# Kernel optimization log

Measured on AMD Instinct MI355X. Metric: run time of the kernel, lower is better.

The kernel has to match this reference:

```python
import jax, jax.numpy as jnp
import numpy as np

N = 50000
E = 800000
IN_DIM = 128
HID = 32
HEADS = 4
NEG_SLOPE = 0.2


def setup_inputs() -> dict:
    key = jax.random.key(0)
    ks = jax.random.split(key, 12)
    x = jax.random.normal(ks[0], (N, IN_DIM), dtype=jnp.float32)
    edge_index = jax.random.randint(ks[1], (2, E), 0, N, dtype=jnp.int64)
    s1 = 1.0 / np.sqrt(IN_DIM)
    s2 = 1.0 / np.sqrt(HEADS * HID)
    W1 = jax.random.normal(ks[2], (IN_DIM, HEADS * HID), dtype=jnp.float32) * s1
    a_src1 = jax.random.normal(ks[3], (HEADS, HID), dtype=jnp.float32) * s1
    a_dst1 = jax.random.normal(ks[4], (HEADS, HID), dtype=jnp.float32) * s1
    b1 = jnp.zeros((HEADS * HID,), dtype=jnp.float32)
    W2 = jax.random.normal(ks[5], (HEADS * HID, HID), dtype=jnp.float32) * s2
    a_src2 = jax.random.normal(ks[6], (1, HID), dtype=jnp.float32) * s2
    a_dst2 = jax.random.normal(ks[7], (1, HID), dtype=jnp.float32) * s2
    b2 = jnp.zeros((HID,), dtype=jnp.float32)
    return {"x": x, "edge_index": edge_index, "W1": W1, "a_src1": a_src1,
            "a_dst1": a_dst1, "b1": b1, "W2": W2, "a_src2": a_src2,
            "a_dst2": a_dst2, "b2": b2}


def _gat_layer(x, W, a_src, a_dst, bias, src, dst, heads, ch):
    n = x.shape[0]
    h = (x @ W).reshape(n, heads, ch)                    # [N,H,C]
    # per-node attention halves (GATv1): a_src . h_i, a_dst . h_j
    al_s = jnp.einsum('nhc,hc->nh', h, a_src)            # [N,H]
    al_d = jnp.einsum('nhc,hc->nh', h, a_dst)
    e = jax.nn.leaky_relu(al_s[src] + al_d[dst], NEG_SLOPE)  # [E,H]
    # segment softmax over edges sharing the same destination
    e_max = jax.ops.segment_max(e, dst, num_segments=n)
    e_exp = jnp.exp(e - e_max[dst])
    denom = jax.ops.segment_sum(e_exp, dst, num_segments=n)
    alpha = e_exp / (denom[dst] + 1e-16)                 # [E,H]
    msg = h[src] * alpha[:, :, None]                     # [E,H,C]
    out = jax.ops.segment_sum(msg, dst, num_segments=n)  # [N,H,C]
    return out.reshape(n, heads * ch) + bias


def reference(x, edge_index, W1, a_src1, a_dst1, b1, W2, a_src2, a_dst2, b2):
    n = x.shape[0]
    # PyG GATConv adds self-loops by default
    loops = jnp.arange(n, dtype=edge_index.dtype)
    src = jnp.concatenate([edge_index[0], loops])
    dst = jnp.concatenate([edge_index[1], loops])
    h = _gat_layer(x, W1, a_src1, a_dst1, b1, src, dst, HEADS, HID)
    h = jax.nn.elu(h)
    out = _gat_layer(h, W2, a_src2, a_dst2, b2, src, dst, 1, HID)
    return out
```

## Files before the change

kernel.cpp:

```cpp
#include <hip/hip_runtime.h>
#include <hip/hip_bf16.h>

#define NN 50000
#define EE 800000
#define EN (EE + NN)
#define IN_DIM 128
#define HID 32
#define HEADS 4
#define F1 (HEADS * HID)
#define NEG 0.2f

typedef __hip_bfloat16 bf16;
typedef __bf16 bf16x8 __attribute__((ext_vector_type(8)));
typedef float f32x4 __attribute__((ext_vector_type(4)));

__device__ __forceinline__ float cvt(float v) { return v; }
__device__ __forceinline__ float cvt(bf16 v)  { return __bfloat162float(v); }

__device__ __forceinline__ float bflo(unsigned u) {
    union { unsigned u; float f; } v; v.u = u << 16; return v.f;
}
__device__ __forceinline__ float bfhi(unsigned u) {
    union { unsigned u; float f; } v; v.u = u & 0xFFFF0000u; return v.f;
}

__device__ __forceinline__ unsigned short f2bf_bits(float f) {
    union { float f; unsigned u; } v; v.f = f;
    unsigned r = v.u + 0x7FFFu + ((v.u >> 16) & 1u);
    return (unsigned short)(r >> 16);
}

__device__ __forceinline__ unsigned short f2h_bits(float f) {
    _Float16 h = (_Float16)f;
    union { _Float16 h; unsigned short s; } v; v.h = h; return v.s;
}
__device__ __forceinline__ float h2f(unsigned short s) {
    union { _Float16 h; unsigned short s; } v; v.s = s; return (float)v.h;
}

__device__ __forceinline__ float rec_exp(uint4 r, int h) {
    unsigned w = (h & 2) ? r.z : r.y;
    unsigned short b = (h & 1) ? (unsigned short)(w >> 16) : (unsigned short)(w & 0xFFFFu);
    return h2f(b);
}

__global__ void k_prep(const void* xv, const void* eiv, const void* W1v, const void* W2v,
                       int* __restrict__ flags,
                       unsigned short* __restrict__ W1T, unsigned short* __restrict__ W2T) {
    __shared__ int sf;
    const int t = threadIdx.x;
    if (t < 64) {
        const unsigned* xw = (const unsigned*)xv;
        const unsigned* ew = (const unsigned*)eiv;
        int lo_nz = 0, huge = 0, hi_nz = 0;
        for (int j = 0; j < 4; ++j) {
            unsigned w = xw[t * 4 + j];
            unsigned lo = w & 0xFFFFu;
            if (lo != 0u) lo_nz = 1;
            if (((lo >> 7) & 0xFFu) >= 0xC0u) huge = 1;
            unsigned eo = ew[(t * 4 + j) * 2 + 1];
            if (eo != 0u) hi_nz = 1;
        }
        unsigned long long m_lo = __ballot(lo_nz);
        unsigned long long m_hg = __ballot(huge);
        unsigned long long m_hi = __ballot(hi_nz);
        if (t == 0) {
            int f0 = (m_lo == 0ull || m_hg != 0ull) ? 1 : 0;
            int f1 = (m_hi == 0ull) ? 1 : 0;
            flags[0] = f0; flags[1] = f1;
            sf = f0;
        }
    }
    __syncthreads();
    const int f32in = sf;
    const unsigned short* w1g = (const unsigned short*)W1v;
    const float* w1f = (const float*)W1v;
    for (int i = 0; i < 64; ++i) {
        int id = i * 256 + t;
        int n = id >> 7, k = id & 127;
        W1T[id] = f32in ? f2bf_bits(w1f[k * 128 + n]) : w1g[k * 128 + n];
    }
    const unsigned short* w2g = (const unsigned short*)W2v;
    const float* w2f = (const float*)W2v;
    for (int i = 0; i < 16; ++i) {
        int id = i * 256 + t;
        int n = id >> 7, k = id & 127;
        W2T[id] = f32in ? f2bf_bits(w2f[k * 32 + n]) : w2g[k * 32 + n];
    }
}

template <typename IT>
__device__ __forceinline__ void get_sd(const IT* __restrict__ ei, int idx, int& s, int& d) {
    if (idx < EE) { s = (int)ei[idx]; d = (int)ei[EE + idx]; }
    else          { s = d = idx - EE; }
}
template <typename IT>
__device__ __forceinline__ int dst_of(const IT* __restrict__ ei, int idx) {
    return idx < EE ? (int)ei[EE + idx] : idx - EE;
}

#define MROWS 64
#define LDK 136

__global__ __launch_bounds__(256) void k_lin1_mfma(
    const void* xv, const unsigned short* __restrict__ W1T,
    const void* as1v, const void* ad1v,
    const int* __restrict__ flags, unsigned* __restrict__ h1,
    float* __restrict__ als, float* __restrict__ ald)
{
    __shared__ __align__(16) char smem[(MROWS + 128) * LDK * 2];
    unsigned short* xs  = (unsigned short*)smem;
    unsigned short* w1t = xs + MROWS * LDK;
    float* hs = (float*)smem;
    __shared__ float sa[F1], sd[F1];

    const int t = threadIdx.x;
    const int row0 = blockIdx.x * MROWS;
    const int f32in = flags[0];

    if (t < F1) {
        sa[t] = f32in ? ((const float*)as1v)[t] : cvt(((const bf16*)as1v)[t]);
        sd[t] = f32in ? ((const float*)ad1v)[t] : cvt(((const bf16*)ad1v)[t]);
    }
    if (!f32in) {
        const uint4* xg = (const uint4*)xv;
        for (int i = 0; i < 4; ++i) {
            int id = i * 256 + t;
            int m = id >> 4, seg = id & 15;
            int gr = row0 + m;
            uint4 val = (gr < NN) ? xg[(size_t)gr * 16 + seg] : make_uint4(0, 0, 0, 0);
            *(uint4*)&xs[m * LDK + seg * 8] = val;
        }
    } else {
        const float* xf = (const float*)xv;
        for (int i = 0; i < 32; ++i) {
            int id = i * 256 + t;
            int m = id >> 7, c = id & 127;
            int gr = row0 + m;
            xs[m * LDK + c] = (gr < NN) ? f2bf_bits(xf[(size_t)gr * 128 + c]) : 0;
        }
    }
    {
        const uint4* wg = (const uint4*)W1T;
        for (int i = 0; i < 8; ++i) {
            int id = i * 256 + t;
            int n = id >> 4, seg = id & 15;
            *(uint4*)&w1t[n * LDK + seg * 8] = wg[id];
        }
    }
    __syncthreads();

    const int wave = t >> 6, lane = t & 63, quad = lane >> 4, l16 = lane & 15;
    f32x4 acc[8];
#pragma unroll
    for (int ni = 0; ni < 8; ++ni) acc[ni] = (f32x4){0.f, 0.f, 0.f, 0.f};

    const int arow = wave * 16 + l16;
#pragma unroll
    for (int kc = 0; kc < 4; ++kc) {
        int ko = kc * 32 + quad * 8;
        bf16x8 av = *(const bf16x8*)&xs[arow * LDK + ko];
#pragma unroll
        for (int ni = 0; ni < 8; ++ni) {
            bf16x8 bv = *(const bf16x8*)&w1t[(ni * 16 + l16) * LDK + ko];
            acc[ni] = __builtin_amdgcn_mfma_f32_16x16x32_bf16(av, bv, acc[ni], 0, 0, 0);
        }
    }
    __syncthreads();

#pragma unroll
    for (int ni = 0; ni < 8; ++ni)
#pragma unroll
        for (int r = 0; r < 4; ++r) {
            int m = wave * 16 + quad * 4 + r;
            hs[m * 132 + ni * 16 + l16] = acc[ni][r];
        }
    __syncthreads();

    for (int i = 0; i < 16; ++i) {
        int id = i * 256 + t;
        int m = id >> 6, wd = id & 63;
        int gr = row0 + m;
        if (gr < NN) {
            unsigned pw = (unsigned)f2bf_bits(hs[m * 132 + 2 * wd]) |
                          ((unsigned)f2bf_bits(hs[m * 132 + 2 * wd + 1]) << 16);
            h1[(size_t)gr * 64 + wd] = pw;
        }
    }
    {
        int m = t >> 2, h = t & 3;
        int gr = row0 + m;
        if (gr < NN) {
            float ps = 0.f, pd = 0.f;
#pragma unroll
            for (int j = 0; j < 32; ++j) {
                float v = hs[m * 132 + h * 32 + j];
                ps += v * sa[h * 32 + j];
                pd += v * sd[h * 32 + j];
            }
            als[gr * 4 + h] = ps;
            ald[gr * 4 + h] = pd;
        }
    }
}

#define SCAN_B 196

__global__ void k_hist(const void* ei, const int* __restrict__ flags,
                       int* __restrict__ counts, int* __restrict__ rank) {
    int idx = blockIdx.x * blockDim.x + threadIdx.x;
    if (idx >= EN) return;
    int d = flags[1] ? dst_of<long long>((const long long*)ei, idx)
                     : dst_of<int>((const int*)ei, idx);
    rank[idx] = atomicAdd(&counts[d], 1);
}

__global__ void k_scanA(const int* __restrict__ counts, int* __restrict__ bsum) {
    __shared__ int sh[256];
    int i = blockIdx.x * 256 + threadIdx.x;
    sh[threadIdx.x] = (i < NN) ? counts[i] : 0;
    __syncthreads();
    for (int off = 128; off > 0; off >>= 1) {
        if (threadIdx.x < off) sh[threadIdx.x] += sh[threadIdx.x + off];
        __syncthreads();
    }
    if (threadIdx.x == 0) bsum[blockIdx.x] = sh[0];
}

__global__ void k_scanC(const int* __restrict__ counts, const int* __restrict__ bsum,
                        int* __restrict__ offsets) {
    __shared__ int red[256];
    __shared__ int sh[256];
    const int t = threadIdx.x, b = blockIdx.x;
    red[t] = (t < b) ? bsum[t] : 0;
    __syncthreads();
    for (int off = 128; off > 0; off >>= 1) {
        if (t < off) red[t] += red[t + off];
        __syncthreads();
    }
    const int base = red[0];
    int i = b * 256 + t;
    int v = (i < NN) ? counts[i] : 0;
    sh[t] = v;
    __syncthreads();
    for (int off = 1; off < 256; off <<= 1) {
        int u = (t >= off) ? sh[t - off] : 0;
        __syncthreads();
        sh[t] += u;
        __syncthreads();
    }
    if (i < NN) {
        offsets[i] = base + sh[t] - v;
    } else if (i == NN) {
        offsets[NN] = EN;
    }
}

__global__ void k_scatter(const void* ei, const int* __restrict__ flags,
                          const int* __restrict__ offsets, const int* __restrict__ rank,
                          const float4* __restrict__ als, const float4* __restrict__ ald,
                          uint4* __restrict__ rec) {
    int idx = blockIdx.x * blockDim.x + threadIdx.x;
    if (idx >= EN) return;
    int s, d;
    if (flags[1]) get_sd<long long>((const long long*)ei, idx, s, d);
    else          get_sd<int>((const int*)ei, idx, s, d);
    int slot = offsets[d] + rank[idx];
    float4 a = als[s], b = ald[d];
    float e0 = a.x + b.x, e1 = a.y + b.y, e2 = a.z + b.z, e3 = a.w + b.w;
    e0 = e0 > 0.f ? e0 : NEG * e0;
    e1 = e1 > 0.f ? e1 : NEG * e1;
    e2 = e2 > 0.f ? e2 : NEG * e2;
    e3 = e3 > 0.f ? e3 : NEG * e3;
    unsigned w0 = (unsigned)f2h_bits(__expf(e0)) | ((unsigned)f2h_bits(__expf(e1)) << 16);
    unsigned w1 = (unsigned)f2h_bits(__expf(e2)) | ((unsigned)f2h_bits(__expf(e3)) << 16);
    rec[slot] = make_uint4((unsigned)s, w0, w1, 0u);
}

__global__ __launch_bounds__(256) void k_agg1(
    const int* __restrict__ offsets, const uint4* __restrict__ rec,
    const bf16* __restrict__ h1, const void* b1v, const int* __restrict__ flags,
    uint2* __restrict__ hm)
{
    const int lane = threadIdx.x & 63;
    const int d = blockIdx.x * 4 + (threadIdx.x >> 6);
    const int q = lane >> 5;
    const int u = lane & 31;
    const int h = u >> 3;
    const int start = offsets[d], end = offsets[d + 1];
    const uint2* rows = (const uint2*)h1;

    float A0[4] = {0,0,0,0}, A1[4] = {0,0,0,0}, A2[4] = {0,0,0,0}, A3[4] = {0,0,0,0};
    float D[4] = {0,0,0,0};
    int e = start + q;
    for (; e + 6 < end; e += 8) {
        uint4 r0 = rec[e],     r1 = rec[e + 2];
        uint4 r2 = rec[e + 4], r3 = rec[e + 6];
        float x0 = rec_exp(r0, h), x1 = rec_exp(r1, h);
        float x2 = rec_exp(r2, h), x3 = rec_exp(r3, h);
        uint2 u0 = rows[r0.x * 32 + u], u1 = rows[r1.x * 32 + u];
        uint2 u2 = rows[r2.x * 32 + u], u3 = rows[r3.x * 32 + u];
        A0[0] += x0 * bflo(u0.x); A0[1] += x0 * bfhi(u0.x);
        A0[2] += x0 * bflo(u0.y); A0[3] += x0 * bfhi(u0.y); D[0] += x0;
        A1[0] += x1 * bflo(u1.x); A1[1] += x1 * bfhi(u1.x);
        A1[2] += x1 * bflo(u1.y); A1[3] += x1 * bfhi(u1.y); D[1] += x1;
        A2[0] += x2 * bflo(u2.x); A2[1] += x2 * bfhi(u2.x);
        A2[2] += x2 * bflo(u2.y); A2[3] += x2 * bfhi(u2.y); D[2] += x2;
        A3[0] += x3 * bflo(u3.x); A3[1] += x3 * bfhi(u3.x);
        A3[2] += x3 * bflo(u3.y); A3[3] += x3 * bfhi(u3.y); D[3] += x3;
    }
    for (; e < end; e += 2) {
        uint4 r0 = rec[e];
        float x0 = rec_exp(r0, h);
        uint2 u0 = rows[r0.x * 32 + u];
        A0[0] += x0 * bflo(u0.x); A0[1] += x0 * bfhi(u0.x);
        A0[2] += x0 * bflo(u0.y); A0[3] += x0 * bfhi(u0.y); D[0] += x0;
    }
    float a0 = A0[0] + A1[0] + A2[0] + A3[0];
    float a1 = A0[1] + A1[1] + A2[1] + A3[1];
    float a2 = A0[2] + A1[2] + A2[2] + A3[2];
    float a3 = A0[3] + A1[3] + A2[3] + A3[3];
    float dsum = D[0] + D[1] + D[2] + D[3];
    a0 += __shfl_xor(a0, 32); a1 += __shfl_xor(a1, 32);
    a2 += __shfl_xor(a2, 32); a3 += __shfl_xor(a3, 32);
    dsum += __shfl_xor(dsum, 32);
    if (q == 0) {
        float inv = 1.f / (dsum + 1e-16f);
        float bb0, bb1, bb2, bb3;
        if (flags[0]) {
            float4 bb = ((const float4*)b1v)[u];
            bb0 = bb.x; bb1 = bb.y; bb2 = bb.z; bb3 = bb.w;
        } else {
            uint2 ub = ((const uint2*)b1v)[u];
            bb0 = bflo(ub.x); bb1 = bfhi(ub.x); bb2 = bflo(ub.y); bb3 = bfhi(ub.y);
        }
        float v0 = a0 * inv + bb0, v1 = a1 * inv + bb1;
        float v2 = a2 * inv + bb2, v3 = a3 * inv + bb3;
        v0 = v0 > 0.f ? v0 : (__expf(v0) - 1.f);
        v1 = v1 > 0.f ? v1 : (__expf(v1) - 1.f);
        v2 = v2 > 0.f ? v2 : (__expf(v2) - 1.f);
        v3 = v3 > 0.f ? v3 : (__expf(v3) - 1.f);
        unsigned w0 = (unsigned)f2bf_bits(v0) | ((unsigned)f2bf_bits(v1) << 16);
        unsigned w1 = (unsigned)f2bf_bits(v2) | ((unsigned)f2bf_bits(v3) << 16);
        hm[(size_t)d * 32 + u] = make_uint2(w0, w1);
    }
}

__global__ __launch_bounds__(256) void k_mid_mfma(
    const bf16* __restrict__ hm, const unsigned short* __restrict__ W2T,
    const void* as2v, const void* ad2v,
    const int* __restrict__ flags, unsigned short* __restrict__ h2,
    float* __restrict__ als2, float* __restrict__ ald2)
{
    __shared__ __align__(16) unsigned short hs[MROWS * LDK];
    __shared__ __align__(16) unsigned short w2t[32 * LDK];
    __shared__ float sa2[HID], sd2[HID];

    const int t = threadIdx.x;
    const int row0 = blockIdx.x * MROWS;
    const int f32in = flags[0];

    if (t < HID) {
        sa2[t] = f32in ? ((const float*)as2v)[t] : cvt(((const bf16*)as2v)[t]);
        sd2[t] = f32in ? ((const float*)ad2v)[t] : cvt(((const bf16*)ad2v)[t]);
    }
    {
        const uint4* hg = (const uint4*)hm;
        for (int i = 0; i < 4; ++i) {
            int id = i * 256 + t;
            int m = id >> 4, seg = id & 15;
            int gr = row0 + m;
            uint4 val = (gr < NN) ? hg[(size_t)gr * 16 + seg] : make_uint4(0, 0, 0, 0);
            *(uint4*)&hs[m * LDK + seg * 8] = val;
        }
        const uint4* wg = (const uint4*)W2T;
        for (int i = 0; i < 2; ++i) {
            int id = i * 256 + t;
            int n = id >> 4, seg = id & 15;
            *(uint4*)&w2t[n * LDK + seg * 8] = wg[id];
        }
    }
    __syncthreads();

    const int wave = t >> 6, lane = t & 63, quad = lane >> 4, l16 = lane & 15;
    f32x4 acc[2];
    acc[0] = (f32x4){0.f, 0.f, 0.f, 0.f};
    acc[1] = (f32x4){0.f, 0.f, 0.f, 0.f};
    const int arow = wave * 16 + l16;
#pragma unroll
    for (int kc = 0; kc < 4; ++kc) {
        int ko = kc * 32 + quad * 8;
        bf16x8 av = *(const bf16x8*)&hs[arow * LDK + ko];
#pragma unroll
        for (int ni = 0; ni < 2; ++ni) {
            bf16x8 bv = *(const bf16x8*)&w2t[(ni * 16 + l16) * LDK + ko];
            acc[ni] = __builtin_amdgcn_mfma_f32_16x16x32_bf16(av, bv, acc[ni], 0, 0, 0);
        }
    }

#pragma unroll
    for (int ni = 0; ni < 2; ++ni)
#pragma unroll
        for (int r = 0; r < 4; ++r) {
            int gr = row0 + wave * 16 + quad * 4 + r;
            if (gr < NN) h2[(size_t)gr * 32 + ni * 16 + l16] = f2h_bits(acc[ni][r]);
        }

    float ps[4], pd[4];
#pragma unroll
    for (int r = 0; r < 4; ++r) {
        ps[r] = acc[0][r] * sa2[l16] + acc[1][r] * sa2[16 + l16];
        pd[r] = acc[0][r] * sd2[l16] + acc[1][r] * sd2[16 + l16];
    }
#pragma unroll
    for (int mask = 1; mask < 16; mask <<= 1)
#pragma unroll
        for (int r = 0; r < 4; ++r) {
            ps[r] += __shfl_xor(ps[r], mask);
            pd[r] += __shfl_xor(pd[r], mask);
        }
    if (l16 == 0) {
#pragma unroll
        for (int r = 0; r < 4; ++r) {
            int gr = row0 + wave * 16 + quad * 4 + r;
            if (gr < NN) { als2[gr] = ps[r]; ald2[gr] = pd[r]; }
        }
    }
}

__global__ __launch_bounds__(256) void k_agg2(
    const int* __restrict__ offsets, const uint4* __restrict__ rec,
    const float* __restrict__ als2, const float* __restrict__ ald2,
    const unsigned* __restrict__ h2,
    const void* b2v, const int* __restrict__ flags, void* out)
{
    const int lane = threadIdx.x & 63;
    const int node = blockIdx.x * 4 + (threadIdx.x >> 6);
    const int q = lane >> 4;
    const int u = lane & 15;
    const int start = offsets[node], end = offsets[node + 1];
    const float adv = ald2[node];

    float A0 = 0.f, A1 = 0.f, B0 = 0.f, B1 = 0.f, D0 = 0.f, D1 = 0.f;
    int e = start + q;
    for (; e + 4 < end; e += 8) {
        int s0 = (int)rec[e].x, s1 = (int)rec[e + 4].x;
        float e0 = als2[s0] + adv, e1 = als2[s1] + adv;
        e0 = e0 > 0.f ? e0 : NEG * e0;
        e1 = e1 > 0.f ? e1 : NEG * e1;
        float x0 = __expf(e0), x1 = __expf(e1);
        unsigned w0 = h2[s0 * 16 + u];
        unsigned w1 = h2[s1 * 16 + u];
        A0 += x0 * h2f((unsigned short)(w0 & 0xFFFFu));
        A1 += x0 * h2f((unsigned short)(w0 >> 16));  D0 += x0;
        B0 += x1 * h2f((unsigned short)(w1 & 0xFFFFu));
        B1 += x1 * h2f((unsigned short)(w1 >> 16));  D1 += x1;
    }
    for (; e < end; e += 4) {
        int s0 = (int)rec[e].x;
        float e0 = als2[s0] + adv;
        e0 = e0 > 0.f ? e0 : NEG * e0;
        float x0 = __expf(e0);
        unsigned w0 = h2[s0 * 16 + u];
        A0 += x0 * h2f((unsigned short)(w0 & 0xFFFFu));
        A1 += x0 * h2f((unsigned short)(w0 >> 16));  D0 += x0;
    }
    float a0 = A0 + B0, a1 = A1 + B1, dsum = D0 + D1;
    a0 += __shfl_xor(a0, 16); a1 += __shfl_xor(a1, 16); dsum += __shfl_xor(dsum, 16);
    a0 += __shfl_xor(a0, 32); a1 += __shfl_xor(a1, 32); dsum += __shfl_xor(dsum, 32);
    if (q == 0) {
        float inv = 1.f / (dsum + 1e-16f);
        float r0 = a0 * inv, r1 = a1 * inv;
        if (flags[0]) {
            float2 bb = ((const float2*)b2v)[u];
            ((float2*)out)[(size_t)node * 16 + u] = make_float2(r0 + bb.x, r1 + bb.y);
        } else {
            unsigned ub = ((const unsigned*)b2v)[u];
            r0 += bflo(ub); r1 += bfhi(ub);
            ((unsigned*)out)[(size_t)node * 16 + u] =
                (unsigned)f2bf_bits(r0) | ((unsigned)f2bf_bits(r1) << 16);
        }
    }
}

extern "C" void kernel_launch(void* const* d_in, const int* in_sizes, int n_in,
                              void* d_out, int out_size, void* d_ws, size_t ws_size,
                              hipStream_t stream) {
    const void* x    = d_in[0];
    const void* ei   = d_in[1];
    const void* W1   = d_in[2];
    const void* a_s1 = d_in[3];
    const void* a_d1 = d_in[4];
    const void* b1   = d_in[5];
    const void* W2   = d_in[6];
    const void* a_s2 = d_in[7];
    const void* a_d2 = d_in[8];
    const void* b2v  = d_in[9];

    int*   flags  = (int*)d_ws;
    char*  pc     = (char*)d_ws + 256;
    uint2* hm     = (uint2*)pc;            pc += (size_t)NN * 32 * 8;
    int*   rank   = (int*)hm;
    bf16*  h1     = (bf16*)pc;             pc += (size_t)NN * F1 * 2;
    unsigned short* h2 = (unsigned short*)h1;
    uint4* rec    = (uint4*)pc;            pc += (size_t)EN * 16;
    float* al_s1  = (float*)pc;            pc += (size_t)NN * HEADS * 4;
    float* al_d1  = (float*)pc;            pc += (size_t)NN * HEADS * 4;
    float* al_s2  = (float*)pc;            pc += (size_t)NN * 4;
    float* al_d2  = (float*)pc;            pc += (size_t)NN * 4;
    int*   offs   = (int*)pc;              pc += (size_t)(NN + 4) * 4;
    int*   counts = (int*)pc;              pc += (size_t)NN * 4;
    unsigned short* W1T = (unsigned short*)pc; pc += (size_t)128 * 128 * 2;
    unsigned short* W2T = (unsigned short*)pc; pc += (size_t)32 * 128 * 2;
    int*   bsum   = (int*)pc;              pc += SCAN_B * 4;

    hipMemsetAsync(counts, 0, (size_t)NN * sizeof(int), stream);

    k_prep<<<1, 256, 0, stream>>>(x, ei, W1, W2, flags, W1T, W2T);
    k_hist<<<(EN + 255) / 256, 256, 0, stream>>>(ei, flags, counts, rank);
    k_scanA<<<SCAN_B, 256, 0, stream>>>(counts, bsum);
    k_scanC<<<SCAN_B, 256, 0, stream>>>(counts, bsum, offs);
    k_lin1_mfma<<<(NN + MROWS - 1) / MROWS, 256, 0, stream>>>(x, W1T, a_s1, a_d1,
                                                              flags, (unsigned*)h1,
                                                              al_s1, al_d1);
    k_scatter<<<(EN + 255) / 256, 256, 0, stream>>>(ei, flags, offs, rank,
                                                    (const float4*)al_s1,
                                                    (const float4*)al_d1, rec);
    k_agg1<<<NN / 4, 256, 0, stream>>>(offs, rec, h1, b1, flags, hm);
    k_mid_mfma<<<(NN + MROWS - 1) / MROWS, 256, 0, stream>>>((const bf16*)hm, W2T, a_s2,
                                                             a_d2, flags, h2, al_s2, al_d2);
    k_agg2<<<NN / 4, 256, 0, stream>>>(offs, rec, al_s2, al_d2, (const unsigned*)h2,
                                       b2v, flags, d_out);
}
```

Before: 261.6 us.

## Pre-pack W1 into MFMA fragment layout and drop LDS staging in lin1

k_prep now writes W1 in the per-lane MFMA B-fragment order, so k_lin1 can load B operands straight from global memory with coalesced uint4 loads. The A fragments are also loaded directly into registers. This removes all LDS staging and syncthreads from the first linear layer. Each block now covers 32 rows, with waves split across row and column halves, and the attention dot products use wave shuffles instead of an LDS pass. The trade-off is scattered 2-byte h1 stores and the W1 fragments being re-read from L2 by every block.

```diff
diff --git a/kernel.cpp b/kernel.cpp
--- a/kernel.cpp
+++ b/kernel.cpp
@@ -46,7 +46,7 @@
 
 __global__ void k_prep(const void* xv, const void* eiv, const void* W1v, const void* W2v,
                        int* __restrict__ flags,
-                       unsigned short* __restrict__ W1T, unsigned short* __restrict__ W2T) {
+                       uint4* __restrict__ W1F, unsigned short* __restrict__ W2T) {
     __shared__ int sf;
     const int t = threadIdx.x;
     if (t < 64) {
@@ -74,11 +74,22 @@
     __syncthreads();
     const int f32in = sf;
     const unsigned short* w1g = (const unsigned short*)W1v;
-    const float* w1f = (const float*)W1v;
-    for (int i = 0; i < 64; ++i) {
-        int id = i * 256 + t;
-        int n = id >> 7, k = id & 127;
-        W1T[id] = f32in ? f2bf_bits(w1f[k * 128 + n]) : w1g[k * 128 + n];
+    const float* w1f32 = (const float*)W1v;
+    for (int i = 0; i < 8; ++i) {
+        int e = i * 256 + t;
+        int nc = e >> 6, lane = e & 63;
+        int ni = nc >> 2, kc = nc & 3, quad = lane >> 4, l16 = lane & 15;
+        int n = ni * 16 + l16, k0 = kc * 32 + quad * 8;
+        unsigned wds[4];
+#pragma unroll
+        for (int p = 0; p < 4; ++p) {
+            unsigned short b0 = f32in ? f2bf_bits(w1f32[(k0 + 2 * p) * 128 + n])
+                                      : w1g[(k0 + 2 * p) * 128 + n];
+            unsigned short b1 = f32in ? f2bf_bits(w1f32[(k0 + 2 * p + 1) * 128 + n])
+                                      : w1g[(k0 + 2 * p + 1) * 128 + n];
+            wds[p] = (unsigned)b0 | ((unsigned)b1 << 16);
+        }
+        W1F[e] = make_uint4(wds[0], wds[1], wds[2], wds[3]);
     }
     const unsigned short* w2g = (const unsigned short*)W2v;
     const float* w2f = (const float*)W2v;
@@ -99,107 +110,103 @@
     return idx < EE ? (int)ei[EE + idx] : idx - EE;
 }
 
-#define MROWS 64
-#define LDK 136
-
 __global__ __launch_bounds__(256) void k_lin1_mfma(
-    const void* xv, const unsigned short* __restrict__ W1T,
+    const void* xv, const uint4* __restrict__ W1F,
     const void* as1v, const void* ad1v,
-    const int* __restrict__ flags, unsigned* __restrict__ h1,
+    const int* __restrict__ flags, unsigned short* __restrict__ h1,
     float* __restrict__ als, float* __restrict__ ald)
 {
-    __shared__ __align__(16) char smem[(MROWS + 128) * LDK * 2];
-    unsigned short* xs  = (unsigned short*)smem;
-    unsigned short* w1t = xs + MROWS * LDK;
-    float* hs = (float*)smem;
-    __shared__ float sa[F1], sd[F1];
-
     const int t = threadIdx.x;
-    const int row0 = blockIdx.x * MROWS;
+    const int w = t >> 6, lane = t & 63, quad = lane >> 4, l16 = lane & 15;
+    const int rhalf = w & 1, chalf = w >> 1;
+    const int row0 = blockIdx.x * 32 + rhalf * 16;
+    const int arow = row0 + l16;
     const int f32in = flags[0];
 
-    if (t < F1) {
-        sa[t] = f32in ? ((const float*)as1v)[t] : cvt(((const bf16*)as1v)[t]);
-        sd[t] = f32in ? ((const float*)ad1v)[t] : cvt(((const bf16*)ad1v)[t]);
-    }
+    uint4 av4[4];
+    const bool okr = arow < NN;
     if (!f32in) {
         const uint4* xg = (const uint4*)xv;
-        for (int i = 0; i < 4; ++i) {
-            int id = i * 256 + t;
-            int m = id >> 4, seg = id & 15;
-            int gr = row0 + m;
-            uint4 val = (gr < NN) ? xg[(size_t)gr * 16 + seg] : make_uint4(0, 0, 0, 0);
-            *(uint4*)&xs[m * LDK + seg * 8] = val;
-        }
+#pragma unroll
+        for (int kc = 0; kc < 4; ++kc)
+            av4[kc] = okr ? xg[(size_t)arow * 16 + kc * 4 + quad]
+                          : make_uint4(0, 0, 0, 0);
     } else {
         const float* xf = (const float*)xv;
-        for (int i = 0; i < 32; ++i) {
-            int id = i * 256 + t;
-            int m = id >> 7, c = id & 127;
-            int gr = row0 + m;
-            xs[m * LDK + c] = (gr < NN) ? f2bf_bits(xf[(size_t)gr * 128 + c]) : 0;
-        }
-    }
-    {
-        const uint4* wg = (const uint4*)W1T;
-        for (int i = 0; i < 8; ++i) {
-            int id = i * 256 + t;
-            int n = id >> 4, seg = id & 15;
-            *(uint4*)&w1t[n * LDK + seg * 8] = wg[id];
-        }
-    }
-    __syncthreads();
-
-    const int wave = t >> 6, lane = t & 63, quad = lane >> 4, l16 = lane & 15;
-    f32x4 acc[8];
-#pragma unroll
-    for (int ni = 0; ni < 8; ++ni) acc[ni] = (f32x4){0.f, 0.f, 0.f, 0.f};
-
-    const int arow = wave * 16 + l16;
+#pragma unroll
+        for (int kc = 0; kc < 4; ++kc) {
+            unsigned wds[4];
+#pragma unroll
+            for (int p = 0; p < 4; ++p) {
+                int k = kc * 32 + quad * 8 + 2 * p;
+                float v0 = okr ? xf[(size_t)arow * 128 + k] : 0.f;
+                float v1 = okr ? xf[(size_t)arow * 128 + k + 1] : 0.f;
+                wds[p] = (unsigned)f2bf_bits(v0) | ((unsigned)f2bf_bits(v1) << 16);
+            }
+            av4[kc] = make_uint4(wds[0], wds[1], wds[2], wds[3]);
+        }
+    }
+
+    f32x4 acc[4];
+#pragma unroll
+    for (int nil = 0; nil < 4; ++nil) acc[nil] = (f32x4){0.f, 0.f, 0.f, 0.f};
 #pragma unroll
     for (int kc = 0; kc < 4; ++kc) {
-        int ko = kc * 32 + quad * 8;
-        bf16x8 av = *(const bf16x8*)&xs[arow * LDK + ko];
-#pragma unroll
-        for (int ni = 0; ni < 8; ++ni) {
-            bf16x8 bv = *(const bf16x8*)&w1t[(ni * 16 + l16) * LDK + ko];
-            acc[ni] = __builtin_amdgcn_mfma_f32_16x16x32_bf16(av, bv, acc[ni], 0, 0, 0);
-        }
-    }
-    __syncthreads();
-
-#pragma unroll
-    for (int ni = 0; ni < 8; ++ni)
+        bf16x8 a = *(bf16x8*)&av4[kc];
+#pragma unroll
+        for (int nil = 0; nil < 4; ++nil) {
+            int nb = chalf * 4 + nil;
+            bf16x8 b = *(const bf16x8*)&W1F[(nb * 4 + kc) * 64 + lane];
+            acc[nil] = __builtin_amdgcn_mfma_f32_16x16x32_bf16(a, b, acc[nil], 0, 0, 0);
+        }
+    }
+
+#pragma unroll
+    for (int nil = 0; nil < 4; ++nil) {
+        int col = (chalf * 4 + nil) * 16 + l16;
 #pragma unroll
         for (int r = 0; r < 4; ++r) {
-            int m = wave * 16 + quad * 4 + r;
-            hs[m * 132 + ni * 16 + l16] = acc[ni][r];
-        }
-    __syncthreads();
-
-    for (int i = 0; i < 16; ++i) {
-        int id = i * 256 + t;
-        int m = id >> 6, wd = id & 63;
-        int gr = row0 + m;
-        if (gr < NN) {
-            unsigned pw = (unsigned)f2bf_bits(hs[m * 132 + 2 * wd]) |
-                          ((unsigned)f2bf_bits(hs[m * 132 + 2 * wd + 1]) << 16);
-            h1[(size_t)gr * 64 + wd] = pw;
-        }
-    }
-    {
-        int m = t >> 2, h = t & 3;
-        int gr = row0 + m;
-        if (gr < NN) {
-            float ps = 0.f, pd = 0.f;
-#pragma unroll
-            for (int j = 0; j < 32; ++j) {
-                float v = hs[m * 132 + h * 32 + j];
-                ps += v * sa[h * 32 + j];
-                pd += v * sd[h * 32 + j];
+            int gr = row0 + quad * 4 + r;
+            if (gr < NN) h1[(size_t)gr * 128 + col] = f2bf_bits(acc[nil][r]);
+        }
+    }
+
+    float saf[4], sdf[4];
+#pragma unroll
+    for (int nil = 0; nil < 4; ++nil) {
+        int col = (chalf * 4 + nil) * 16 + l16;
+        saf[nil] = f32in ? ((const float*)as1v)[col] : cvt(((const bf16*)as1v)[col]);
+        sdf[nil] = f32in ? ((const float*)ad1v)[col] : cvt(((const bf16*)ad1v)[col]);
+    }
+    float ps[2][4], pd[2][4];
+#pragma unroll
+    for (int hi = 0; hi < 2; ++hi)
+#pragma unroll
+        for (int r = 0; r < 4; ++r) {
+            ps[hi][r] = acc[2 * hi][r] * saf[2 * hi] + acc[2 * hi + 1][r] * saf[2 * hi + 1];
+            pd[hi][r] = acc[2 * hi][r] * sdf[2 * hi] + acc[2 * hi + 1][r] * sdf[2 * hi + 1];
+        }
+#pragma unroll
+    for (int mask = 1; mask < 16; mask <<= 1)
+#pragma unroll
+        for (int hi = 0; hi < 2; ++hi)
+#pragma unroll
+            for (int r = 0; r < 4; ++r) {
+                ps[hi][r] += __shfl_xor(ps[hi][r], mask);
+                pd[hi][r] += __shfl_xor(pd[hi][r], mask);
             }
-            als[gr * 4 + h] = ps;
-            ald[gr * 4 + h] = pd;
+    if (l16 == 0) {
+#pragma unroll
+        for (int hi = 0; hi < 2; ++hi) {
+            int h = chalf * 2 + hi;
+#pragma unroll
+            for (int r = 0; r < 4; ++r) {
+                int gr = row0 + quad * 4 + r;
+                if (gr < NN) {
+                    als[gr * 4 + h] = ps[hi][r];
+                    ald[gr * 4 + h] = pd[hi][r];
+                }
+            }
         }
     }
 }
@@ -346,6 +353,9 @@
     }
 }
 
+#define MROWS 64
+#define LDK 136
+
 __global__ __launch_bounds__(256) void k_mid_mfma(
     const bf16* __restrict__ hm, const unsigned short* __restrict__ W2T,
     const void* as2v, const void* ad2v,
@@ -510,19 +520,18 @@
     float* al_d2  = (float*)pc;            pc += (size_t)NN * 4;
     int*   offs   = (int*)pc;              pc += (size_t)(NN + 4) * 4;
     int*   counts = (int*)pc;              pc += (size_t)NN * 4;
-    unsigned short* W1T = (unsigned short*)pc; pc += (size_t)128 * 128 * 2;
+    uint4* W1F    = (uint4*)pc;            pc += (size_t)2048 * 16;
     unsigned short* W2T = (unsigned short*)pc; pc += (size_t)32 * 128 * 2;
     int*   bsum   = (int*)pc;              pc += SCAN_B * 4;
 
     hipMemsetAsync(counts, 0, (size_t)NN * sizeof(int), stream);
 
-    k_prep<<<1, 256, 0, stream>>>(x, ei, W1, W2, flags, W1T, W2T);
+    k_prep<<<1, 256, 0, stream>>>(x, ei, W1, W2, flags, W1F, W2T);
     k_hist<<<(EN + 255) / 256, 256, 0, stream>>>(ei, flags, counts, rank);
     k_scanA<<<SCAN_B, 256, 0, stream>>>(counts, bsum);
     k_scanC<<<SCAN_B, 256, 0, stream>>>(counts, bsum, offs);
-    k_lin1_mfma<<<(NN + MROWS - 1) / MROWS, 256, 0, stream>>>(x, W1T, a_s1, a_d1,
-                                                              flags, (unsigned*)h1,
-                                                              al_s1, al_d1);
+    k_lin1_mfma<<<(NN + 31) / 32, 256, 0, stream>>>(x, W1F, a_s1, a_d1, flags,
+                                                    (unsigned short*)h1, al_s1, al_d1);
     k_scatter<<<(EN + 255) / 256, 256, 0, stream>>>(ei, flags, offs, rank,
                                                     (const float4*)al_s1,
                                                     (const float4*)al_d1, rec);
```

Measured after the change: 268.8 us. +2.8%, slower.
